# Kernel optimization log

Hardware: AMD Instinct MI355X
Metric: run time of the kernel (lower is better)

## Reference

```python
import jax, jax.numpy as jnp
import numpy as np

N_NODES = 100000
N_EDGES = 1600000


def setup_inputs() -> dict:
    key = jax.random.key(0)
    ks = jax.random.split(key, 5)
    x = jax.random.normal(ks[0], (N_NODES, 128), dtype=jnp.float32)
    edge_index = jax.random.randint(ks[1], (2, N_EDGES), 0, N_NODES, dtype=jnp.int64)
    edge_weight = jnp.ones((N_EDGES,), dtype=jnp.float32)
    W1 = jax.random.normal(ks[2], (128, 128), dtype=jnp.float32) * (1.0 / np.sqrt(128))
    b1 = jnp.zeros((128,), dtype=jnp.float32)
    W2 = jax.random.normal(ks[3], (128, 64), dtype=jnp.float32) * (1.0 / np.sqrt(128))
    b2 = jnp.zeros((64,), dtype=jnp.float32)
    return {"x": x, "edge_index": edge_index, "edge_weight": edge_weight,
            "W1": W1, "b1": b1, "W2": W2, "b2": b2}


def _gcn_conv(x, rows, cols, W, b, n_nodes):
    # GCNConv(normalize=True), unit edge weights (forward overwrites weights with ones)
    h = x @ W                                             # [N, out]
    ones_w = jnp.ones(rows.shape[0], dtype=x.dtype)
    deg = jax.ops.segment_sum(ones_w, cols, num_segments=n_nodes)   # in-degree at targets
    dinv = jnp.where(deg > 0, deg ** -0.5, 0.0)
    norm = dinv[rows] * dinv[cols]                        # [E+N]
    msg = h[rows] * norm[:, None]                         # gather + scale, memory-bound
    out = jax.ops.segment_sum(msg, cols, num_segments=n_nodes)
    return out + b


def reference(x, edge_index, edge_weight, W1, b1, W2, b2):
    n = x.shape[0]
    loop = jnp.arange(n, dtype=edge_index.dtype)
    rows = jnp.concatenate([edge_index[0], loop])         # self-loops (PyG default)
    cols = jnp.concatenate([edge_index[1], loop])
    h = jax.nn.relu(_gcn_conv(x, rows, cols, W1, b1, n))
    logits = _gcn_conv(h, rows, cols, W2, b2, n)
    return logits
```

## Files before the change

### kernel.cpp

```cpp
#include <hip/hip_runtime.h>
#include <hip/hip_fp16.h>


constexpr int NN = 100000;
constexpr int NE = 1600000;
constexpr int BSH = 7;
constexpr int NB = (NN + 127) >> BSH;
constexpr int NBLK = 256;
constexpr int EPB = NE / NBLK;
constexpr int TSTR = 784;

typedef _Float16 f16x8 __attribute__((ext_vector_type(8)));
typedef float f32x4 __attribute__((ext_vector_type(4)));

__global__ __launch_bounds__(256) void k_histwt(const int* __restrict__ cols,
                                                int* __restrict__ table,
                                                const float* __restrict__ W1,
                                                const float* __restrict__ W2,
                                                __half* __restrict__ Wt1,
                                                __half* __restrict__ Wt2) {
  if (blockIdx.x < NBLK) {
    __shared__ int cnt[NB];
    for (int i = threadIdx.x; i < NB; i += 256) cnt[i] = 0;
    __syncthreads();
    int base = blockIdx.x * EPB;
    for (int i = threadIdx.x; i < EPB; i += 256)
      atomicAdd(&cnt[cols[base + i] >> BSH], 1);
    __syncthreads();
    for (int i = threadIdx.x; i < NB; i += 256)
      table[blockIdx.x * TSTR + i] = cnt[i];
  } else {
    int i = (blockIdx.x - NBLK) * 256 + threadIdx.x;
    if (i < 16384) {
      int k = i >> 7, n = i & 127;
      Wt1[n * 128 + k] = __float2half(W1[i]);
    } else {
      int j = i - 16384;
      int k = j >> 6, n = j & 63;
      Wt2[n * 128 + k] = __float2half(W2[j]);
    }
  }
}

__global__ __launch_bounds__(256) void k_scanT(const int* __restrict__ table,
                                               int* __restrict__ startOff,
                                               int* __restrict__ btot) {
  __shared__ int s[256];
  int b = blockIdx.x, t = threadIdx.x;
  int v = table[t * TSTR + b];
  s[t] = v;
  __syncthreads();
  for (int off = 1; off < 256; off <<= 1) {
    int tmp = (t >= off) ? s[t - off] : 0;
    __syncthreads();
    s[t] += tmp;
    __syncthreads();
  }
  startOff[t * TSTR + b] = s[t] - v;
  if (t == 255) btot[b] = s[t];
}

__global__ __launch_bounds__(256) void k_scatB(const int* __restrict__ rows,
                                               const int* __restrict__ cols,
                                               const int* __restrict__ startOff,
                                               const int* __restrict__ btot,
                                               int* __restrict__ bucketBase,
                                               unsigned* __restrict__ binned) {
  __shared__ int bb[NB];
  __shared__ int s[256];
  __shared__ int scnt[NB];
  int tid = threadIdx.x;
  int base4 = tid * 4;
  int d0 = (base4 + 0 < NB) ? btot[base4 + 0] : 0;
  int d1 = (base4 + 1 < NB) ? btot[base4 + 1] : 0;
  int d2 = (base4 + 2 < NB) ? btot[base4 + 2] : 0;
  int d3 = (base4 + 3 < NB) ? btot[base4 + 3] : 0;
  int tsum = d0 + d1 + d2 + d3;
  s[tid] = tsum;
  __syncthreads();
  for (int off = 1; off < 256; off <<= 1) {
    int tmp = (tid >= off) ? s[tid - off] : 0;
    __syncthreads();
    s[tid] += tmp;
    __syncthreads();
  }
  int ex = s[tid] - tsum;
  if (base4 + 0 < NB) bb[base4 + 0] = ex;
  if (base4 + 1 < NB) bb[base4 + 1] = ex + d0;
  if (base4 + 2 < NB) bb[base4 + 2] = ex + d0 + d1;
  if (base4 + 3 < NB) bb[base4 + 3] = ex + d0 + d1 + d2;
  __syncthreads();
  if (blockIdx.x == 0)
    for (int i = tid; i < NB; i += 256) bucketBase[i] = bb[i];
  for (int i = tid; i < NB; i += 256)
    scnt[i] = bb[i] + startOff[blockIdx.x * TSTR + i];
  __syncthreads();
  int base = blockIdx.x * EPB;
  for (int i = tid; i < EPB; i += 256) {
    int c = cols[base + i];
    int r = rows[base + i];
    int pos = atomicAdd(&scnt[c >> BSH], 1);
    binned[pos] = ((unsigned)r << BSH) | (unsigned)(c & 127);
  }
}

__global__ __launch_bounds__(256) void k_fillb(const unsigned* __restrict__ binned,
                                               const int* __restrict__ bucketBase,
                                               const int* __restrict__ btot,
                                               int* __restrict__ rowptr,
                                               int* __restrict__ deg,
                                               float* __restrict__ dinv,
                                               int* __restrict__ srcIdx,
                                               const float4* __restrict__ x4,
                                               float2* __restrict__ y8) {
  __shared__ int cnt[128];
  __shared__ int sc[128];
  __shared__ int rp[128];
  __shared__ float sdv[128];
  int b = blockIdx.x;
  int nb0 = b << BSH;
  int nn = min(128, NN - nb0);
  int tid = threadIdx.x;
  if (tid < 128) cnt[tid] = 0;
  __syncthreads();
  int ebeg = bucketBase[b];
  int eend = ebeg + btot[b];
  for (int p = ebeg + tid; p < eend; p += 256)
    atomicAdd(&cnt[binned[p] & 127], 1);
  __syncthreads();
  int v = (tid < 128) ? cnt[tid] : 0;
  if (tid < 128) sc[tid] = v;
  __syncthreads();
  for (int off = 1; off < 128; off <<= 1) {
    int tmp = (tid < 128 && tid >= off) ? sc[tid - off] : 0;
    __syncthreads();
    if (tid < 128) sc[tid] += tmp;
    __syncthreads();
  }
  if (tid < 128) {
    int ex = sc[tid] - v;
    rp[tid] = ebeg + ex;
    float dv = rsqrtf((float)v + 1.0f);
    sdv[tid] = dv;
    if (tid < nn) {
      rowptr[nb0 + tid] = ebeg + ex;
      deg[nb0 + tid] = v;
      dinv[nb0 + tid] = dv;
    }
    cnt[tid] = 0;
  }
  __syncthreads();
  for (int p = ebeg + tid; p < eend; p += 256) {
    unsigned pk = binned[p];
    int cl = pk & 127;
    int local = atomicAdd(&cnt[cl], 1);
    srcIdx[rp[cl] + local] = (int)(pk >> BSH);
  }
  int tot = nn << 5;
  const float4* xb = x4 + ((size_t)nb0 << 5);
  float2* yb = y8 + ((size_t)nb0 << 5);
  for (int i = tid; i < tot; i += 256) {
    float sfac = sdv[i >> 5];
    float4 vv = xb[i];
    union { __half2 h[2]; float2 f; } u;
    u.h[0] = __floats2half2_rn(vv.x * sfac, vv.y * sfac);
    u.h[1] = __floats2half2_rn(vv.z * sfac, vv.w * sfac);
    yb[i] = u.f;
  }
}

__global__ __launch_bounds__(256, 8) void k_fused(
    const __half* __restrict__ y, const int* __restrict__ rowptr,
    const int* __restrict__ deg, const int* __restrict__ srcIdx,
    const float* __restrict__ dinv, const __half* __restrict__ Wt1,
    const float* __restrict__ b1, const __half* __restrict__ Wt2,
    __half* __restrict__ z) {
  __shared__ __align__(16) __half sA[16][136];
  __shared__ __align__(16) __half sB[16][136];
  const int w = threadIdx.x >> 6, l = threadIdx.x & 63;
  const int blk0 = blockIdx.x * 16;
  const int quad = l >> 4, m = l & 15;

  int hd = 0, hp = 0;
  float hv = 0.0f;
  if (l < 4) {
    hd = deg[blk0 + w * 4 + l];
    hp = rowptr[blk0 + w * 4 + l];
    hv = dinv[blk0 + w * 4 + l];
  }
  int d = __shfl(hd, 0);
  int ptr = __shfl(hp, 0);
  int my = (l < min(d, 64)) ? srcIdx[ptr + l] : 0;

  for (int i = 0; i < 4; ++i) {
    const int node = blk0 + w * 4 + i;
    const int dn = (i < 3) ? __shfl(hd, i + 1) : 0;
    const int pn = (i < 3) ? __shfl(hp, i + 1) : 0;
    int myn = (i < 3 && l < min(dn, 64)) ? srcIdx[pn + l] : 0;
    f16x8 sv = *reinterpret_cast<const f16x8*>(y + (size_t)node * 128 + m * 8);

    float acc[8];
#pragma unroll
    for (int j = 0; j < 8; j++) acc[j] = 0.0f;

    {
      int cnt = min(d, 64);
      int k = 0;
      for (; k + 16 <= cnt; k += 16) {
        int s0 = __shfl(my, k + quad);
        int s1 = __shfl(my, k + 4 + quad);
        int s2 = __shfl(my, k + 8 + quad);
        int s3 = __shfl(my, k + 12 + quad);
        f16x8 v0 = *reinterpret_cast<const f16x8*>(y + (size_t)s0 * 128 + m * 8);
        f16x8 v1 = *reinterpret_cast<const f16x8*>(y + (size_t)s1 * 128 + m * 8);
        f16x8 v2 = *reinterpret_cast<const f16x8*>(y + (size_t)s2 * 128 + m * 8);
        f16x8 v3 = *reinterpret_cast<const f16x8*>(y + (size_t)s3 * 128 + m * 8);
#pragma unroll
        for (int j = 0; j < 8; j++) acc[j] += (float)v0[j];
#pragma unroll
        for (int j = 0; j < 8; j++) acc[j] += (float)v1[j];
#pragma unroll
        for (int j = 0; j < 8; j++) acc[j] += (float)v2[j];
#pragma unroll
        for (int j = 0; j < 8; j++) acc[j] += (float)v3[j];
      }
      for (; k + 8 <= cnt; k += 8) {
        int s0 = __shfl(my, k + quad);
        int s1 = __shfl(my, k + 4 + quad);
        f16x8 v0 = *reinterpret_cast<const f16x8*>(y + (size_t)s0 * 128 + m * 8);
        f16x8 v1 = *reinterpret_cast<const f16x8*>(y + (size_t)s1 * 128 + m * 8);
#pragma unroll
        for (int j = 0; j < 8; j++) acc[j] += (float)v0[j];
#pragma unroll
        for (int j = 0; j < 8; j++) acc[j] += (float)v1[j];
      }
      for (; k < cnt; k += 4) {
        int idx = k + quad;
        bool valid = idx < cnt;
        int s0 = __shfl(my, valid ? idx : 0);
        f16x8 v0 = *reinterpret_cast<const f16x8*>(y + (size_t)s0 * 128 + m * 8);
        if (valid) {
#pragma unroll
          for (int j = 0; j < 8; j++) acc[j] += (float)v0[j];
        }
      }
    }
    for (int base = 64; base < d; base += 64) {
      int cnt = min(64, d - base);
      int mt = (l < cnt) ? srcIdx[ptr + base + l] : 0;
      int k = 0;
      for (; k + 8 <= cnt; k += 8) {
        int s0 = __shfl(mt, k + quad);
        int s1 = __shfl(mt, k + 4 + quad);
        f16x8 v0 = *reinterpret_cast<const f16x8*>(y + (size_t)s0 * 128 + m * 8);
        f16x8 v1 = *reinterpret_cast<const f16x8*>(y + (size_t)s1 * 128 + m * 8);
#pragma unroll
        for (int j = 0; j < 8; j++) acc[j] += (float)v0[j];
#pragma unroll
        for (int j = 0; j < 8; j++) acc[j] += (float)v1[j];
      }
      for (; k < cnt; k += 4) {
        int idx = k + quad;
        bool valid = idx < cnt;
        int s0 = __shfl(mt, valid ? idx : 0);
        f16x8 v0 = *reinterpret_cast<const f16x8*>(y + (size_t)s0 * 128 + m * 8);
        if (valid) {
#pragma unroll
          for (int j = 0; j < 8; j++) acc[j] += (float)v0[j];
        }
      }
    }

#pragma unroll
    for (int j = 0; j < 8; j++) acc[j] += __shfl_xor(acc[j], 16);
#pragma unroll
    for (int j = 0; j < 8; j++) acc[j] += __shfl_xor(acc[j], 32);
    if (quad == 0) {
      float scn = __shfl(hv, i);
      f16x8 o;
#pragma unroll
      for (int j = 0; j < 8; j++)
        o[j] = (_Float16)((acc[j] + (float)sv[j]) * scn);
      *reinterpret_cast<f16x8*>(&sA[w * 4 + i][m * 8]) = o;
    }
    d = dn;
    ptr = pn;
    my = myn;
  }
  __syncthreads();

  f16x8 afrag[4];
#pragma unroll
  for (int kk = 0; kk < 4; kk++)
    afrag[kk] = *reinterpret_cast<const f16x8*>(&sA[m][kk * 32 + quad * 8]);
  f32x4 acc1[2];
#pragma unroll
  for (int t = 0; t < 2; t++) {
    float bv = b1[(w * 2 + t) * 16 + m];
    acc1[t] = (f32x4){bv, bv, bv, bv};
  }
#pragma unroll
  for (int kk = 0; kk < 4; kk++) {
#pragma unroll
    for (int t = 0; t < 2; t++) {
      f16x8 b = *reinterpret_cast<const f16x8*>(
          Wt1 + (size_t)((w * 2 + t) * 16 + m) * 128 + kk * 32 + quad * 8);
      acc1[t] = __builtin_amdgcn_mfma_f32_16x16x32_f16(afrag[kk], b, acc1[t], 0, 0, 0);
    }
  }
#pragma unroll
  for (int t = 0; t < 2; t++)
#pragma unroll
    for (int i = 0; i < 4; i++)
      sB[quad * 4 + i][(w * 2 + t) * 16 + m] =
          __float2half(fmaxf(acc1[t][i], 0.0f));
  __syncthreads();

  f16x8 hfrag[4];
#pragma unroll
  for (int kk = 0; kk < 4; kk++)
    hfrag[kk] = *reinterpret_cast<const f16x8*>(&sB[m][kk * 32 + quad * 8]);
  f32x4 acc2 = (f32x4){0.f, 0.f, 0.f, 0.f};
#pragma unroll
  for (int kk = 0; kk < 4; kk++) {
    f16x8 b = *reinterpret_cast<const f16x8*>(
        Wt2 + (size_t)(w * 16 + m) * 128 + kk * 32 + quad * 8);
    acc2 = __builtin_amdgcn_mfma_f32_16x16x32_f16(hfrag[kk], b, acc2, 0, 0, 0);
  }
  float rs[4];
#pragma unroll
  for (int i = 0; i < 4; i++) rs[i] = dinv[blk0 + quad * 4 + i];
#pragma unroll
  for (int i = 0; i < 4; i++)
    sA[quad * 4 + i][w * 16 + m] = __float2half(acc2[i] * rs[i]);
  __syncthreads();

  if (threadIdx.x < 128) {
    int r = threadIdx.x >> 3, cc = threadIdx.x & 7;
    *reinterpret_cast<float4*>(z + (size_t)(blk0 + r) * 64 + cc * 8) =
        *reinterpret_cast<const float4*>(&sA[r][cc * 8]);
  }
}

__global__ __launch_bounds__(256) void k_gath2(const __half* __restrict__ z,
                                               const int* __restrict__ rowptr,
                                               const int* __restrict__ deg,
                                               const int* __restrict__ srcIdx,
                                               const float* __restrict__ dinv,
                                               const float* __restrict__ b2,
                                               float* __restrict__ out) {
  int node = blockIdx.x * 4 + (threadIdx.x >> 6);
  if (node >= NN) return;
  int lane = threadIdx.x & 63;
  int g = lane >> 3;
  int c = lane & 7;
  int d = deg[node];
  int p = rowptr[node];
  size_t coff = (size_t)c * 8;
  float acc[8];
#pragma unroll
  for (int i = 0; i < 8; i++) acc[i] = 0.0f;

  for (int base = 0; base < d; base += 64) {
    int cnt = min(64, d - base);
    int my = (lane < cnt) ? srcIdx[p + base + lane] : 0;
    int k = 0;
    for (; k + 32 <= cnt; k += 32) {
      int s0 = __shfl(my, k + g);
      int s1 = __shfl(my, k + 8 + g);
      int s2 = __shfl(my, k + 16 + g);
      int s3 = __shfl(my, k + 24 + g);
      f16x8 v0 = *reinterpret_cast<const f16x8*>(z + (size_t)s0 * 64 + coff);
      f16x8 v1 = *reinterpret_cast<const f16x8*>(z + (size_t)s1 * 64 + coff);
      f16x8 v2 = *reinterpret_cast<const f16x8*>(z + (size_t)s2 * 64 + coff);
      f16x8 v3 = *reinterpret_cast<const f16x8*>(z + (size_t)s3 * 64 + coff);
#pragma unroll
      for (int i = 0; i < 8; i++) acc[i] += (float)v0[i];
#pragma unroll
      for (int i = 0; i < 8; i++) acc[i] += (float)v1[i];
#pragma unroll
      for (int i = 0; i < 8; i++) acc[i] += (float)v2[i];
#pragma unroll
      for (int i = 0; i < 8; i++) acc[i] += (float)v3[i];
    }
    for (; k + 16 <= cnt; k += 16) {
      int s0 = __shfl(my, k + g);
      int s1 = __shfl(my, k + 8 + g);
      f16x8 v0 = *reinterpret_cast<const f16x8*>(z + (size_t)s0 * 64 + coff);
      f16x8 v1 = *reinterpret_cast<const f16x8*>(z + (size_t)s1 * 64 + coff);
#pragma unroll
      for (int i = 0; i < 8; i++) acc[i] += (float)v0[i];
#pragma unroll
      for (int i = 0; i < 8; i++) acc[i] += (float)v1[i];
    }
    for (; k < cnt; k += 8) {
      int idx = k + g;
      bool valid = idx < cnt;
      int s0 = __shfl(my, valid ? idx : 0);
      f16x8 v0 = *reinterpret_cast<const f16x8*>(z + (size_t)s0 * 64 + coff);
      if (valid) {
#pragma unroll
        for (int i = 0; i < 8; i++) acc[i] += (float)v0[i];
      }
    }
  }
#pragma unroll
  for (int i = 0; i < 8; i++) acc[i] += __shfl_xor(acc[i], 8);
#pragma unroll
  for (int i = 0; i < 8; i++) acc[i] += __shfl_xor(acc[i], 16);
#pragma unroll
  for (int i = 0; i < 8; i++) acc[i] += __shfl_xor(acc[i], 32);
  if (g == 0) {
    f16x8 sv = *reinterpret_cast<const f16x8*>(z + (size_t)node * 64 + coff);
    float s = dinv[node];
    const float4* b4 = reinterpret_cast<const float4*>(b2);
    float4 bv0 = b4[2 * c], bv1 = b4[2 * c + 1];
    float4 o0, o1;
    o0.x = (acc[0] + (float)sv[0]) * s + bv0.x;
    o0.y = (acc[1] + (float)sv[1]) * s + bv0.y;
    o0.z = (acc[2] + (float)sv[2]) * s + bv0.z;
    o0.w = (acc[3] + (float)sv[3]) * s + bv0.w;
    o1.x = (acc[4] + (float)sv[4]) * s + bv1.x;
    o1.y = (acc[5] + (float)sv[5]) * s + bv1.y;
    o1.z = (acc[6] + (float)sv[6]) * s + bv1.z;
    o1.w = (acc[7] + (float)sv[7]) * s + bv1.w;
    float4* op = reinterpret_cast<float4*>(out + (size_t)node * 64 + coff);
    op[0] = o0;
    op[1] = o1;
  }
}

extern "C" void kernel_launch(void* const* d_in, const int* in_sizes, int n_in,
                              void* d_out, int out_size, void* d_ws, size_t ws_size,
                              hipStream_t stream) {
  const float* x  = (const float*)d_in[0];
  const int*   ei = (const int*)d_in[1];
  const int* rows = ei;
  const int* cols = ei + NE;
  const float* W1 = (const float*)d_in[3];
  const float* b1 = (const float*)d_in[4];
  const float* W2 = (const float*)d_in[5];
  const float* b2 = (const float*)d_in[6];
  float* out = (float*)d_out;

  char* base = (char*)d_ws;
  constexpr size_t MB = 1 << 20;
  int*      deg       = (int*)(base + 0 * MB);
  int*      rowptr    = (int*)(base + 1 * MB);
  float*    dinv      = (float*)(base + 2 * MB);
  int*      btot      = (int*)(base + 3 * MB);
  int*      bucketBase= (int*)(base + 3 * MB + 16 * 1024);
  __half*   Wt1       = (__half*)(base + 3 * MB + 64 * 1024);
  __half*   Wt2       = (__half*)(base + 3 * MB + 128 * 1024);
  int*      table     = (int*)(base + 4 * MB);
  int*      startOff  = (int*)(base + 5 * MB);
  unsigned* binned    = (unsigned*)(base + 6 * MB);
  int*      srcIdx    = (int*)(base + 13 * MB);
  __half*   y         = (__half*)(base + 20 * MB);
  __half*   z         = (__half*)(base + 46 * MB);

  k_histwt<<<NBLK + 96, 256, 0, stream>>>(cols, table, W1, W2, Wt1, Wt2);
  k_scanT<<<NB, 256, 0, stream>>>(table, startOff, btot);
  k_scatB<<<NBLK, 256, 0, stream>>>(rows, cols, startOff, btot, bucketBase,
                                    binned);
  k_fillb<<<NB, 256, 0, stream>>>(binned, bucketBase, btot, rowptr, deg, dinv,
                                  srcIdx, (const float4*)x, (float2*)y);
  k_fused<<<NN / 16, 256, 0, stream>>>(y, rowptr, deg, srcIdx, dinv,
                                       Wt1, b1, Wt2, z);
  k_gath2<<<(NN + 3) / 4, 256, 0, stream>>>(z, rowptr, deg, srcIdx, dinv, b2, out);
}
```

Before: 284.3 us.

## Widen histogram/scatter to 800 blocks and use half-wave per node in layer-2 gather

Raises the number of edge-partition blocks for the histogram and binned scatter from 256 to 800, so these phases spread across more CUs. The column scan is adapted to have each thread handle four rows, and workspace offsets are moved to fit the larger table. The layer-2 gather now assigns 32 lanes per node instead of 64, handling two nodes per wavefront. With an average degree of about 16 this leaves fewer idle lanes and drops one cross-lane reduction step, at the cost of less memory-level parallelism for high-degree nodes.

```diff
diff --git a/kernel.cpp b/kernel.cpp
--- a/kernel.cpp
+++ b/kernel.cpp
@@ -6,7 +6,7 @@
 constexpr int NE = 1600000;
 constexpr int BSH = 7;
 constexpr int NB = (NN + 127) >> BSH;
-constexpr int NBLK = 256;
+constexpr int NBLK = 800;
 constexpr int EPB = NE / NBLK;
 constexpr int TSTR = 784;
 
@@ -47,8 +47,13 @@
                                                int* __restrict__ btot) {
   __shared__ int s[256];
   int b = blockIdx.x, t = threadIdx.x;
-  int v = table[t * TSTR + b];
-  s[t] = v;
+  int r0 = t * 4;
+  int v0 = (r0 + 0 < NBLK) ? table[(size_t)(r0 + 0) * TSTR + b] : 0;
+  int v1 = (r0 + 1 < NBLK) ? table[(size_t)(r0 + 1) * TSTR + b] : 0;
+  int v2 = (r0 + 2 < NBLK) ? table[(size_t)(r0 + 2) * TSTR + b] : 0;
+  int v3 = (r0 + 3 < NBLK) ? table[(size_t)(r0 + 3) * TSTR + b] : 0;
+  int tsum = v0 + v1 + v2 + v3;
+  s[t] = tsum;
   __syncthreads();
   for (int off = 1; off < 256; off <<= 1) {
     int tmp = (t >= off) ? s[t - off] : 0;
@@ -56,8 +61,12 @@
     s[t] += tmp;
     __syncthreads();
   }
-  startOff[t * TSTR + b] = s[t] - v;
-  if (t == 255) btot[b] = s[t];
+  int ex = s[t] - tsum;
+  if (r0 + 0 < NBLK) startOff[(size_t)(r0 + 0) * TSTR + b] = ex;
+  if (r0 + 1 < NBLK) startOff[(size_t)(r0 + 1) * TSTR + b] = ex + v0;
+  if (r0 + 2 < NBLK) startOff[(size_t)(r0 + 2) * TSTR + b] = ex + v0 + v1;
+  if (r0 + 3 < NBLK) startOff[(size_t)(r0 + 3) * TSTR + b] = ex + v0 + v1 + v2;
+  if (t == 255) btot[b] = s[255];
 }
 
 __global__ __launch_bounds__(256) void k_scatB(const int* __restrict__ rows,
@@ -93,7 +102,7 @@
   if (blockIdx.x == 0)
     for (int i = tid; i < NB; i += 256) bucketBase[i] = bb[i];
   for (int i = tid; i < NB; i += 256)
-    scnt[i] = bb[i] + startOff[blockIdx.x * TSTR + i];
+    scnt[i] = bb[i] + startOff[(size_t)blockIdx.x * TSTR + i];
   __syncthreads();
   int base = blockIdx.x * EPB;
   for (int i = tid; i < EPB; i += 256) {
@@ -349,11 +358,14 @@
                                                const float* __restrict__ dinv,
                                                const float* __restrict__ b2,
                                                float* __restrict__ out) {
-  int node = blockIdx.x * 4 + (threadIdx.x >> 6);
+  const int lane = threadIdx.x & 63;
+  const int h = lane >> 5;
+  const int l5 = lane & 31;
+  const int g = l5 >> 3;
+  const int c = l5 & 7;
+  const int h32 = h << 5;
+  int node = blockIdx.x * 8 + ((threadIdx.x >> 6) << 1) + h;
   if (node >= NN) return;
-  int lane = threadIdx.x & 63;
-  int g = lane >> 3;
-  int c = lane & 7;
   int d = deg[node];
   int p = rowptr[node];
   size_t coff = (size_t)c * 8;
@@ -361,15 +373,15 @@
 #pragma unroll
   for (int i = 0; i < 8; i++) acc[i] = 0.0f;
 
-  for (int base = 0; base < d; base += 64) {
-    int cnt = min(64, d - base);
-    int my = (lane < cnt) ? srcIdx[p + base + lane] : 0;
+  for (int base = 0; base < d; base += 32) {
+    int cnt = min(32, d - base);
+    int my = (l5 < cnt) ? srcIdx[p + base + l5] : 0;
     int k = 0;
-    for (; k + 32 <= cnt; k += 32) {
-      int s0 = __shfl(my, k + g);
-      int s1 = __shfl(my, k + 8 + g);
-      int s2 = __shfl(my, k + 16 + g);
-      int s3 = __shfl(my, k + 24 + g);
+    for (; k + 16 <= cnt; k += 16) {
+      int s0 = __shfl(my, h32 + k + g);
+      int s1 = __shfl(my, h32 + k + 4 + g);
+      int s2 = __shfl(my, h32 + k + 8 + g);
+      int s3 = __shfl(my, h32 + k + 12 + g);
       f16x8 v0 = *reinterpret_cast<const f16x8*>(z + (size_t)s0 * 64 + coff);
       f16x8 v1 = *reinterpret_cast<const f16x8*>(z + (size_t)s1 * 64 + coff);
       f16x8 v2 = *reinterpret_cast<const f16x8*>(z + (size_t)s2 * 64 + coff);
@@ -383,9 +395,9 @@
 #pragma unroll
       for (int i = 0; i < 8; i++) acc[i] += (float)v3[i];
     }
-    for (; k + 16 <= cnt; k += 16) {
-      int s0 = __shfl(my, k + g);
-      int s1 = __shfl(my, k + 8 + g);
+    for (; k + 8 <= cnt; k += 8) {
+      int s0 = __shfl(my, h32 + k + g);
+      int s1 = __shfl(my, h32 + k + 4 + g);
       f16x8 v0 = *reinterpret_cast<const f16x8*>(z + (size_t)s0 * 64 + coff);
       f16x8 v1 = *reinterpret_cast<const f16x8*>(z + (size_t)s1 * 64 + coff);
 #pragma unroll
@@ -393,10 +405,10 @@
 #pragma unroll
       for (int i = 0; i < 8; i++) acc[i] += (float)v1[i];
     }
-    for (; k < cnt; k += 8) {
+    for (; k < cnt; k += 4) {
       int idx = k + g;
       bool valid = idx < cnt;
-      int s0 = __shfl(my, valid ? idx : 0);
+      int s0 = __shfl(my, h32 + (valid ? idx : 0));
       f16x8 v0 = *reinterpret_cast<const f16x8*>(z + (size_t)s0 * 64 + coff);
       if (valid) {
 #pragma unroll
@@ -408,8 +420,6 @@
   for (int i = 0; i < 8; i++) acc[i] += __shfl_xor(acc[i], 8);
 #pragma unroll
   for (int i = 0; i < 8; i++) acc[i] += __shfl_xor(acc[i], 16);
-#pragma unroll
-  for (int i = 0; i < 8; i++) acc[i] += __shfl_xor(acc[i], 32);
   if (g == 0) {
     f16x8 sv = *reinterpret_cast<const f16x8*>(z + (size_t)node * 64 + coff);
     float s = dinv[node];
@@ -453,11 +463,11 @@
   __half*   Wt1       = (__half*)(base + 3 * MB + 64 * 1024);
   __half*   Wt2       = (__half*)(base + 3 * MB + 128 * 1024);
   int*      table     = (int*)(base + 4 * MB);
-  int*      startOff  = (int*)(base + 5 * MB);
-  unsigned* binned    = (unsigned*)(base + 6 * MB);
-  int*      srcIdx    = (int*)(base + 13 * MB);
-  __half*   y         = (__half*)(base + 20 * MB);
-  __half*   z         = (__half*)(base + 46 * MB);
+  int*      startOff  = (int*)(base + 7 * MB);
+  unsigned* binned    = (unsigned*)(base + 10 * MB);
+  int*      srcIdx    = (int*)(base + 17 * MB);
+  __half*   y         = (__half*)(base + 24 * MB);
+  __half*   z         = (__half*)(base + 50 * MB);
 
   k_histwt<<<NBLK + 96, 256, 0, stream>>>(cols, table, W1, W2, Wt1, Wt2);
   k_scanT<<<NB, 256, 0, stream>>>(table, startOff, btot);
@@ -467,5 +477,5 @@
                                   srcIdx, (const float4*)x, (float2*)y);
   k_fused<<<NN / 16, 256, 0, stream>>>(y, rowptr, deg, srcIdx, dinv,
                                        Wt1, b1, Wt2, z);
-  k_gath2<<<(NN + 3) / 4, 256, 0, stream>>>(z, rowptr, deg, srcIdx, dinv, b2, out);
-}
+  k_gath2<<<(NN + 7) / 8, 256, 0, stream>>>(z, rowptr, deg, srcIdx, dinv, b2, out);
+}
```

Measured after the change: 288.5 us. About the same (+1.5%).
